# Optimization experiments

Measured on AMD Instinct MI355X. Metric: run time of the kernel, lower is better.

Reference implementation:

```python
import jax, jax.numpy as jnp
import numpy as np

N, F_IN, F_OUT = 8192, 256, 128
ALPHA = 0.2  # LeakyReLU negative slope
NEG_BIG = -9e15


def setup_inputs() -> dict:
    key = jax.random.key(0)
    k1, k2, k3, k4 = jax.random.split(key, 4)
    h = jax.random.normal(k1, (N, F_IN), dtype=jnp.float32)
    adj = jax.random.randint(k2, (N, N), 0, 2, dtype=jnp.int32)
    # Xavier-uniform-ish scaled params (gain 1.414)
    w_bound = 1.414 * np.sqrt(6.0 / (F_IN + F_OUT))
    a_bound = 1.414 * np.sqrt(6.0 / (2 * F_OUT + 1))
    W = jax.random.uniform(k3, (F_IN, F_OUT), jnp.float32, -w_bound, w_bound)
    a = jax.random.uniform(k4, (2 * F_OUT, 1), jnp.float32, -a_bound, a_bound)
    return {"h": h, "adj": adj, "W": W, "a": a}


def reference(h, adj, W, a):
    # Wh: [N, F_OUT]
    Wh = h @ W
    # a = [a1; a2]; e_ij = leakyrelu(a1.Wh_i + a2.Wh_j) == the torch concat+matmul,
    # computed via broadcast-add instead of materializing [N, N, 2F].
    a1 = a[:F_OUT, 0]   # [F_OUT]
    a2 = a[F_OUT:, 0]   # [F_OUT]
    si = Wh @ a1        # [N]
    sj = Wh @ a2        # [N]
    e = jax.nn.leaky_relu(si[:, None] + sj[None, :], negative_slope=ALPHA)  # [N, N]
    logits = jnp.where(adj > 0, e, NEG_BIG)
    attention = jax.nn.softmax(logits, axis=1)
    # dropout is identity in eval mode (training=False)
    h_prime = attention @ Wh  # [N, F_OUT]
    return jax.nn.elu(h_prime)  # concat=True path
```

## Files before the change

kernel.cpp:

```cpp
#include <hip/hip_runtime.h>

#define NN 8192
#define FIN 256
#define FOUT 128
#define BKJ 128
#define LALPHA 0.2f

typedef short bf16x8 __attribute__((ext_vector_type(8)));
typedef float f32x4 __attribute__((ext_vector_type(4)));

#define FOR8(X) X(0) X(1) X(2) X(3) X(4) X(5) X(6) X(7)

static __device__ __forceinline__ unsigned short f2bf(float f) {
    unsigned u = __float_as_uint(f);
    u += 0x7FFFu + ((u >> 16) & 1u);
    return (unsigned short)(u >> 16);
}
static __device__ __forceinline__ float bf2f(unsigned short b) {
    return __uint_as_float(((unsigned)b) << 16);
}

__global__ __launch_bounds__(256) void gat_k1(
    const float* __restrict__ h, const float* __restrict__ W,
    const float* __restrict__ a, unsigned short* __restrict__ WhT,
    float* __restrict__ si, float* __restrict__ sj)
{
    __shared__ float Wt[64 * 128];
    __shared__ float hT[64 * 36 + 4];
    const int t = threadIdx.x;
    const int r0 = blockIdx.x * 32;
    const int rg = t >> 5;
    const int cg = t & 31;
    float acc[4][4] = {{0.f,0.f,0.f,0.f},{0.f,0.f,0.f,0.f},{0.f,0.f,0.f,0.f},{0.f,0.f,0.f,0.f}};

    for (int kc = 0; kc < 4; ++kc) {
        __syncthreads();
        const float4* Ws = (const float4*)(W + kc * 64 * FOUT);
        float4* Wd = (float4*)Wt;
        #pragma unroll
        for (int v = 0; v < 8; ++v) Wd[v * 256 + t] = Ws[v * 256 + t];
        {
            const int hr = t >> 3, hk = (t & 7) * 8;
            const float* hs = h + (size_t)(r0 + hr) * FIN + kc * 64 + hk;
            float4 x0 = *(const float4*)hs;
            float4 x1 = *(const float4*)(hs + 4);
            hT[(hk + 0) * 36 + hr] = x0.x; hT[(hk + 1) * 36 + hr] = x0.y;
            hT[(hk + 2) * 36 + hr] = x0.z; hT[(hk + 3) * 36 + hr] = x0.w;
            hT[(hk + 4) * 36 + hr] = x1.x; hT[(hk + 5) * 36 + hr] = x1.y;
            hT[(hk + 6) * 36 + hr] = x1.z; hT[(hk + 7) * 36 + hr] = x1.w;
        }
        __syncthreads();
        #pragma unroll 8
        for (int kk = 0; kk < 64; ++kk) {
            float4 hv4 = *(const float4*)&hT[kk * 36 + rg * 4];
            float4 wv4 = *(const float4*)&Wt[kk * 128 + cg * 4];
            float hv[4] = {hv4.x, hv4.y, hv4.z, hv4.w};
            float wv[4] = {wv4.x, wv4.y, wv4.z, wv4.w};
            #pragma unroll
            for (int rr = 0; rr < 4; ++rr)
                #pragma unroll
                for (int cc = 0; cc < 4; ++cc)
                    acc[rr][cc] = fmaf(hv[rr], wv[cc], acc[rr][cc]);
        }
    }
    float4 a1v4 = *(const float4*)(a + cg * 4);
    float4 a2v4 = *(const float4*)(a + FOUT + cg * 4);
    float a1v[4] = {a1v4.x, a1v4.y, a1v4.z, a1v4.w};
    float a2v[4] = {a2v4.x, a2v4.y, a2v4.z, a2v4.w};
    float ps[4], qs[4];
    #pragma unroll
    for (int rr = 0; rr < 4; ++rr) {
        float p = 0.f, q = 0.f;
        #pragma unroll
        for (int cc = 0; cc < 4; ++cc) {
            p = fmaf(acc[rr][cc], a1v[cc], p);
            q = fmaf(acc[rr][cc], a2v[cc], q);
        }
        ps[rr] = p; qs[rr] = q;
    }
    #pragma unroll
    for (int off = 1; off <= 16; off <<= 1) {
        #pragma unroll
        for (int rr = 0; rr < 4; ++rr) {
            ps[rr] += __shfl_xor(ps[rr], off);
            qs[rr] += __shfl_xor(qs[rr], off);
        }
    }
    if (cg == 0) {
        #pragma unroll
        for (int rr = 0; rr < 4; ++rr) {
            si[r0 + rg * 4 + rr] = ps[rr];
            sj[r0 + rg * 4 + rr] = qs[rr];
        }
    }
    #pragma unroll
    for (int cc = 0; cc < 4; ++cc) {
        ushort4 v;
        v.x = f2bf(acc[0][cc]); v.y = f2bf(acc[1][cc]);
        v.z = f2bf(acc[2][cc]); v.w = f2bf(acc[3][cc]);
        *(ushort4*)(WhT + (size_t)(cg * 4 + cc) * NN + r0 + rg * 4) = v;
    }
}

__global__ __launch_bounds__(256) void gat_k1s(
    const float* __restrict__ sj, float* __restrict__ sjmax)
{
    __shared__ float red[256];
    float m = -1e30f;
    for (int i = threadIdx.x; i < NN; i += 256) m = fmaxf(m, sj[i]);
    red[threadIdx.x] = m;
    __syncthreads();
    for (int o = 128; o > 0; o >>= 1) {
        if (threadIdx.x < o) red[threadIdx.x] = fmaxf(red[threadIdx.x], red[threadIdx.x + o]);
        __syncthreads();
    }
    if (threadIdx.x == 0) sjmax[0] = red[0];
}

static __device__ __forceinline__ unsigned short pcalc(
    int a, float sjv, float si_l, float m_row, float& ls)
{
    float x = si_l + sjv;
    x = fmaxf(x, LALPHA * x);
    float p = (a > 0) ? __expf(x - m_row) : 0.f;
    unsigned short pb = f2bf(p);
    ls += bf2f(pb);
    return pb;
}

template<int JS, bool FINAL>
__global__ __launch_bounds__(256, 2) void gat_k2(
    const int* __restrict__ adj, const unsigned short* __restrict__ WhT,
    const float* __restrict__ si, const float* __restrict__ sj,
    const float* __restrict__ sjmaxp,
    float* __restrict__ lsum, float* __restrict__ Opart, float* __restrict__ out)
{
    const int JR_ = NN / JS;
    const int NST_ = JR_ / BKJ;
    __shared__ __align__(16) unsigned short tile[2][16384];
    const int t = threadIdx.x;
    const int w = t >> 6, l = t & 63;
    const int rb = (int)blockIdx.x / JS, js = (int)blockIdx.x % JS;
    const int iw = rb * 64 + w * 16;
    const int j0 = js * JR_;
    const int row = l & 15, kg = l >> 4;

    const float si_l = si[iw + row];
    const float sjmax = sjmaxp[0];
    const float xm = si_l + sjmax;
    const float m_row = fmaxf(xm, LALPHA * xm);
    const float* sjb = sj + j0 + kg * 8;
    const int c_row = t >> 4, ch = t & 15;
    const int* adjb = adj + (size_t)(iw + row) * NN + j0 + kg * 8;

#define GSRC_D(v) const unsigned short* gsrc##v = WhT + (size_t)(v * 16 + c_row) * NN + j0 + ch * 8; \
                  const int ldo##v = ((v * 256 + t) * 16) ^ ((c_row & 7) << 4);
    FOR8(GSRC_D)

#define REG_D(v) int4 stg##v, adr##v;
    FOR8(REG_D)

#define STG_L0(v) stg##v = *(const int4*)(gsrc##v);
    FOR8(STG_L0)
#define ADR_L0(q) adr##q = *(const int4*)(adjb + (q / 2) * 32 + (q % 2) * 4);
    FOR8(ADR_L0)

#define ACC_D(n) f32x4 acc##n = {0.f, 0.f, 0.f, 0.f};
    FOR8(ACC_D)
    float ls = 0.f;
    const int kg16 = kg * 16;

#define STG_WR(v) *(int4*)((char*)tb + ldo##v) = stg##v;
#define STG_LN(v) stg##v = *(const int4*)(gsrc##v + so);
#define ADR_LN(q) adr##q = *(const int4*)(adjb + so + (q / 2) * 32 + (q % 2) * 4);
#define P8(AF, A0, A1, sp) { \
    float4 s0_ = *(const float4*)(sp); float4 s1_ = *(const float4*)((sp) + 4); \
    AF[0] = (short)pcalc(A0.x, s0_.x, si_l, m_row, ls); \
    AF[1] = (short)pcalc(A0.y, s0_.y, si_l, m_row, ls); \
    AF[2] = (short)pcalc(A0.z, s0_.z, si_l, m_row, ls); \
    AF[3] = (short)pcalc(A0.w, s0_.w, si_l, m_row, ls); \
    AF[4] = (short)pcalc(A1.x, s1_.x, si_l, m_row, ls); \
    AF[5] = (short)pcalc(A1.y, s1_.y, si_l, m_row, ls); \
    AF[6] = (short)pcalc(A1.z, s1_.z, si_l, m_row, ls); \
    AF[7] = (short)pcalc(A1.w, s1_.w, si_l, m_row, ls); }
#define MFMA_ROW(n) { const int c_ = n * 16 + row; \
    const int off_ = c_ * 256 + (KB ^ ((c_ & 7) << 4)); \
    bf16x8 bv_ = *(const bf16x8*)((const char*)tb + off_); \
    acc##n = __builtin_amdgcn_mfma_f32_16x16x32_bf16(AFk, bv_, acc##n, 0, 0, 0); }
#define MFMA_KC(afv, kcl) { const bf16x8 AFk = afv; const int KB = kcl * 64 + kg16; FOR8(MFMA_ROW) }

    for (int s = 0; s < NST_; ++s) {
        unsigned short* tb = tile[s & 1];
        FOR8(STG_WR)
        if (s + 1 < NST_) {
            const size_t so = (size_t)(s + 1) * BKJ;
            FOR8(STG_LN)
        }
        bf16x8 af0, af1, af2, af3;
        {
            const float* spp = sjb + s * BKJ;
            P8(af0, adr0, adr1, spp)
            P8(af1, adr2, adr3, spp + 32)
            P8(af2, adr4, adr5, spp + 64)
            P8(af3, adr6, adr7, spp + 96)
        }
        if (s + 1 < NST_) {
            const size_t so = (size_t)(s + 1) * BKJ;
            FOR8(ADR_LN)
        }
        __syncthreads();
        MFMA_KC(af0, 0) MFMA_KC(af1, 1) MFMA_KC(af2, 2) MFMA_KC(af3, 3)
    }

    ls += __shfl_xor(ls, 16);
    ls += __shfl_xor(ls, 32);
    if (FINAL) {
        float lsr0 = __shfl(ls, kg * 4 + 0);
        float lsr1 = __shfl(ls, kg * 4 + 1);
        float lsr2 = __shfl(ls, kg * 4 + 2);
        float lsr3 = __shfl(ls, kg * 4 + 3);
#define FN_ROW(n) { size_t ob = (size_t)(iw + kg * 4) * FOUT + n * 16 + row; \
    float o0 = acc##n[0] / lsr0; out[ob]            = (o0 > 0.f) ? o0 : expm1f(o0); \
    float o1 = acc##n[1] / lsr1; out[ob + FOUT]     = (o1 > 0.f) ? o1 : expm1f(o1); \
    float o2 = acc##n[2] / lsr2; out[ob + 2 * FOUT] = (o2 > 0.f) ? o2 : expm1f(o2); \
    float o3 = acc##n[3] / lsr3; out[ob + 3 * FOUT] = (o3 > 0.f) ? o3 : expm1f(o3); }
        FOR8(FN_ROW)
    } else {
        if (l < 16) lsum[(size_t)js * NN + iw + l] = ls;
#define ST_ROW(n) { size_t ob = ((size_t)js * NN + iw + kg * 4) * FOUT + n * 16 + row; \
    Opart[ob] = acc##n[0]; Opart[ob + FOUT] = acc##n[1]; \
    Opart[ob + 2 * FOUT] = acc##n[2]; Opart[ob + 3 * FOUT] = acc##n[3]; }
        FOR8(ST_ROW)
    }
}

__global__ __launch_bounds__(256) void gat_k3(
    const float* __restrict__ lsum, const float* __restrict__ Opart,
    float* __restrict__ out)
{
    const int t = threadIdx.x;
    const int i = (int)blockIdx.x * 2 + (t >> 7);
    const int f = t & 127;
    float den = lsum[i] + lsum[NN + i] + lsum[2 * NN + i] + lsum[3 * NN + i];
    size_t base = (size_t)i * FOUT + f;
    const size_t SP = (size_t)NN * FOUT;
    float num = Opart[base] + Opart[SP + base]
              + Opart[2 * SP + base] + Opart[3 * SP + base];
    float o = num / den;
    out[base] = (o > 0.f) ? o : expm1f(o);
}

extern "C" void kernel_launch(void* const* d_in, const int* in_sizes, int n_in,
                              void* d_out, int out_size, void* d_ws, size_t ws_size,
                              hipStream_t stream) {
    const float* h  = (const float*)d_in[0];
    const int*  adj = (const int*)d_in[1];
    const float* W  = (const float*)d_in[2];
    const float* a  = (const float*)d_in[3];
    float* out = (float*)d_out;
    char* ws = (char*)d_ws;
    unsigned short* WhT = (unsigned short*)ws;
    float* si     = (float*)(ws + 2097152);
    float* sj     = (float*)(ws + 2129920);
    float* sjmax  = (float*)(ws + 2162688);
    float* lsum   = (float*)(ws + 2162944);
    float* Opart  = (float*)(ws + 2294016);
    const size_t need4 = 2294016 + (size_t)4 * NN * FOUT * 4;

    gat_k1<<<256, 256, 0, stream>>>(h, W, a, WhT, si, sj);
    gat_k1s<<<1, 256, 0, stream>>>(sj, sjmax);
    if (ws_size >= need4) {
        gat_k2<4, false><<<512, 256, 0, stream>>>(adj, WhT, si, sj, sjmax, lsum, Opart, out);
        gat_k3<<<4096, 256, 0, stream>>>(lsum, Opart, out);
    } else {
        gat_k2<1, true><<<128, 256, 0, stream>>>(adj, WhT, si, sj, sjmax, lsum, Opart, out);
    }
}
```

Before: 98.58 us.

## Load WhT MFMA operands directly from global memory, removing LDS tile staging

Drops the double-buffered shared-memory tile and __syncthreads. Each lane now loads its B-fragments of WhT straight from global memory into registers, split into two batches around the softmax-probability computation. The row-sum accumulator is split into four independent partial sums to shorten the dependency chain. This removes LDS traffic and block-wide barriers but makes each wave fetch WhT separately (4 waves per block now load the same data), uses more VGPRs, and relies on L2/L1 hits.

```diff
diff --git a/kernel.cpp b/kernel.cpp
--- a/kernel.cpp
+++ b/kernel.cpp
@@ -137,7 +137,6 @@
 {
     const int JR_ = NN / JS;
     const int NST_ = JR_ / BKJ;
-    __shared__ __align__(16) unsigned short tile[2][16384];
     const int t = threadIdx.x;
     const int w = t >> 6, l = t & 63;
     const int rb = (int)blockIdx.x / JS, js = (int)blockIdx.x % JS;
@@ -150,68 +149,66 @@
     const float xm = si_l + sjmax;
     const float m_row = fmaxf(xm, LALPHA * xm);
     const float* sjb = sj + j0 + kg * 8;
-    const int c_row = t >> 4, ch = t & 15;
     const int* adjb = adj + (size_t)(iw + row) * NN + j0 + kg * 8;
 
-#define GSRC_D(v) const unsigned short* gsrc##v = WhT + (size_t)(v * 16 + c_row) * NN + j0 + ch * 8; \
-                  const int ldo##v = ((v * 256 + t) * 16) ^ ((c_row & 7) << 4);
-    FOR8(GSRC_D)
-
-#define REG_D(v) int4 stg##v, adr##v;
-    FOR8(REG_D)
-
-#define STG_L0(v) stg##v = *(const int4*)(gsrc##v);
-    FOR8(STG_L0)
+#define WB_D(n) const unsigned short* wb##n = WhT + (size_t)(n * 16 + row) * NN + j0 + kg * 8;
+    FOR8(WB_D)
+
+#define ADR_D(q) int4 adr##q;
+    FOR8(ADR_D)
 #define ADR_L0(q) adr##q = *(const int4*)(adjb + (q / 2) * 32 + (q % 2) * 4);
     FOR8(ADR_L0)
 
 #define ACC_D(n) f32x4 acc##n = {0.f, 0.f, 0.f, 0.f};
     FOR8(ACC_D)
-    float ls = 0.f;
-    const int kg16 = kg * 16;
-
-#define STG_WR(v) *(int4*)((char*)tb + ldo##v) = stg##v;
-#define STG_LN(v) stg##v = *(const int4*)(gsrc##v + so);
+    float ls0 = 0.f, ls1 = 0.f, ls2 = 0.f, ls3 = 0.f;
+
 #define ADR_LN(q) adr##q = *(const int4*)(adjb + so + (q / 2) * 32 + (q % 2) * 4);
-#define P8(AF, A0, A1, sp) { \
+#define P8(AF, A0, A1, sp, LSV) { \
     float4 s0_ = *(const float4*)(sp); float4 s1_ = *(const float4*)((sp) + 4); \
-    AF[0] = (short)pcalc(A0.x, s0_.x, si_l, m_row, ls); \
-    AF[1] = (short)pcalc(A0.y, s0_.y, si_l, m_row, ls); \
-    AF[2] = (short)pcalc(A0.z, s0_.z, si_l, m_row, ls); \
-    AF[3] = (short)pcalc(A0.w, s0_.w, si_l, m_row, ls); \
-    AF[4] = (short)pcalc(A1.x, s1_.x, si_l, m_row, ls); \
-    AF[5] = (short)pcalc(A1.y, s1_.y, si_l, m_row, ls); \
-    AF[6] = (short)pcalc(A1.z, s1_.z, si_l, m_row, ls); \
-    AF[7] = (short)pcalc(A1.w, s1_.w, si_l, m_row, ls); }
-#define MFMA_ROW(n) { const int c_ = n * 16 + row; \
-    const int off_ = c_ * 256 + (KB ^ ((c_ & 7) << 4)); \
-    bf16x8 bv_ = *(const bf16x8*)((const char*)tb + off_); \
-    acc##n = __builtin_amdgcn_mfma_f32_16x16x32_bf16(AFk, bv_, acc##n, 0, 0, 0); }
-#define MFMA_KC(afv, kcl) { const bf16x8 AFk = afv; const int KB = kcl * 64 + kg16; FOR8(MFMA_ROW) }
-
+    AF[0] = (short)pcalc(A0.x, s0_.x, si_l, m_row, LSV); \
+    AF[1] = (short)pcalc(A0.y, s0_.y, si_l, m_row, LSV); \
+    AF[2] = (short)pcalc(A0.z, s0_.z, si_l, m_row, LSV); \
+    AF[3] = (short)pcalc(A0.w, s0_.w, si_l, m_row, LSV); \
+    AF[4] = (short)pcalc(A1.x, s1_.x, si_l, m_row, LSV); \
+    AF[5] = (short)pcalc(A1.y, s1_.y, si_l, m_row, LSV); \
+    AF[6] = (short)pcalc(A1.z, s1_.z, si_l, m_row, LSV); \
+    AF[7] = (short)pcalc(A1.w, s1_.w, si_l, m_row, LSV); }
+#define FG_L0(n) int4 fg0##n = *(const int4*)(wb##n + sofs);
+#define FG_L1(n) int4 fg1##n = *(const int4*)(wb##n + sofs + 32);
+#define FG_L2(n) int4 fg2##n = *(const int4*)(wb##n + sofs + 64);
+#define FG_L3(n) int4 fg3##n = *(const int4*)(wb##n + sofs + 96);
+#define MM0(n) acc##n = __builtin_amdgcn_mfma_f32_16x16x32_bf16(af0, *(const bf16x8*)&fg0##n, acc##n, 0, 0, 0);
+#define MM1(n) acc##n = __builtin_amdgcn_mfma_f32_16x16x32_bf16(af1, *(const bf16x8*)&fg1##n, acc##n, 0, 0, 0);
+#define MM2(n) acc##n = __builtin_amdgcn_mfma_f32_16x16x32_bf16(af2, *(const bf16x8*)&fg2##n, acc##n, 0, 0, 0);
+#define MM3(n) acc##n = __builtin_amdgcn_mfma_f32_16x16x32_bf16(af3, *(const bf16x8*)&fg3##n, acc##n, 0, 0, 0);
+
+    #pragma unroll 1
     for (int s = 0; s < NST_; ++s) {
-        unsigned short* tb = tile[s & 1];
-        FOR8(STG_WR)
-        if (s + 1 < NST_) {
-            const size_t so = (size_t)(s + 1) * BKJ;
-            FOR8(STG_LN)
-        }
+        const size_t sofs = (size_t)s * BKJ;
+        FOR8(FG_L0)
+        FOR8(FG_L1)
         bf16x8 af0, af1, af2, af3;
         {
             const float* spp = sjb + s * BKJ;
-            P8(af0, adr0, adr1, spp)
-            P8(af1, adr2, adr3, spp + 32)
-            P8(af2, adr4, adr5, spp + 64)
-            P8(af3, adr6, adr7, spp + 96)
+            P8(af0, adr0, adr1, spp,      ls0)
+            P8(af1, adr2, adr3, spp + 32, ls1)
+            P8(af2, adr4, adr5, spp + 64, ls2)
+            P8(af3, adr6, adr7, spp + 96, ls3)
         }
         if (s + 1 < NST_) {
             const size_t so = (size_t)(s + 1) * BKJ;
             FOR8(ADR_LN)
         }
-        __syncthreads();
-        MFMA_KC(af0, 0) MFMA_KC(af1, 1) MFMA_KC(af2, 2) MFMA_KC(af3, 3)
-    }
-
+        FOR8(FG_L2)
+        FOR8(FG_L3)
+        FOR8(MM0)
+        FOR8(MM1)
+        FOR8(MM2)
+        FOR8(MM3)
+    }
+
+    float ls = (ls0 + ls1) + (ls2 + ls3);
     ls += __shfl_xor(ls, 16);
     ls += __shfl_xor(ls, 32);
     if (FINAL) {
```

Result: slower. 184.3 us (+86.9%).

## Halve j-tile, double split-K to 8, compute row sums via MFMA with ones

Applied to the files above, without the earlier changes.

Shrinks the per-stage j tile from 128 to 64 to halve LDS and register staging, which allows four blocks per CU, and doubles the j-split to eight so 1024 blocks cover the GPU. The softmax denominator is no longer accumulated with scalar adds and shuffles. It comes from an extra MFMA against a vector of bf16 ones, taking VALU work off the exp path. The trade-off is twice as much partial-output traffic written and then reduced in gat_k3, plus a larger workspace.

```diff
diff --git a/kernel.cpp b/kernel.cpp
--- a/kernel.cpp
+++ b/kernel.cpp
@@ -3,21 +3,20 @@
 #define NN 8192
 #define FIN 256
 #define FOUT 128
-#define BKJ 128
+#define BKJ 64
+#define JSPLIT 8
 #define LALPHA 0.2f
 
 typedef short bf16x8 __attribute__((ext_vector_type(8)));
 typedef float f32x4 __attribute__((ext_vector_type(4)));
 
 #define FOR8(X) X(0) X(1) X(2) X(3) X(4) X(5) X(6) X(7)
+#define FOR4(X) X(0) X(1) X(2) X(3)
 
 static __device__ __forceinline__ unsigned short f2bf(float f) {
     unsigned u = __float_as_uint(f);
     u += 0x7FFFu + ((u >> 16) & 1u);
     return (unsigned short)(u >> 16);
-}
-static __device__ __forceinline__ float bf2f(unsigned short b) {
-    return __uint_as_float(((unsigned)b) << 16);
 }
 
 __global__ __launch_bounds__(256) void gat_k1(
@@ -118,18 +117,16 @@
 }
 
 static __device__ __forceinline__ unsigned short pcalc(
-    int a, float sjv, float si_l, float m_row, float& ls)
+    int a, float sjv, float si_l, float m_row)
 {
     float x = si_l + sjv;
     x = fmaxf(x, LALPHA * x);
     float p = (a > 0) ? __expf(x - m_row) : 0.f;
-    unsigned short pb = f2bf(p);
-    ls += bf2f(pb);
-    return pb;
+    return f2bf(p);
 }
 
 template<int JS, bool FINAL>
-__global__ __launch_bounds__(256, 2) void gat_k2(
+__global__ __launch_bounds__(256, 4) void gat_k2(
     const int* __restrict__ adj, const unsigned short* __restrict__ WhT,
     const float* __restrict__ si, const float* __restrict__ sj,
     const float* __restrict__ sjmaxp,
@@ -137,7 +134,7 @@
 {
     const int JR_ = NN / JS;
     const int NST_ = JR_ / BKJ;
-    __shared__ __align__(16) unsigned short tile[2][16384];
+    __shared__ __align__(16) unsigned short tile[2][8192];
     const int t = threadIdx.x;
     const int w = t >> 6, l = t & 63;
     const int rb = (int)blockIdx.x / JS, js = (int)blockIdx.x % JS;
@@ -150,24 +147,25 @@
     const float xm = si_l + sjmax;
     const float m_row = fmaxf(xm, LALPHA * xm);
     const float* sjb = sj + j0 + kg * 8;
-    const int c_row = t >> 4, ch = t & 15;
     const int* adjb = adj + (size_t)(iw + row) * NN + j0 + kg * 8;
 
-#define GSRC_D(v) const unsigned short* gsrc##v = WhT + (size_t)(v * 16 + c_row) * NN + j0 + ch * 8; \
-                  const int ldo##v = ((v * 256 + t) * 16) ^ ((c_row & 7) << 4);
-    FOR8(GSRC_D)
+#define GSRC_D(v) const unsigned short* gsrc##v = WhT + (size_t)(v * 32 + (t >> 3)) * NN + j0 + (t & 7) * 8; \
+                  const int ldo##v = ((v * 256 + t) * 16) ^ (((t >> 3) & 7) << 4);
+    FOR4(GSRC_D)
 
 #define REG_D(v) int4 stg##v, adr##v;
-    FOR8(REG_D)
-
+    FOR4(REG_D)
 #define STG_L0(v) stg##v = *(const int4*)(gsrc##v);
-    FOR8(STG_L0)
+    FOR4(STG_L0)
 #define ADR_L0(q) adr##q = *(const int4*)(adjb + (q / 2) * 32 + (q % 2) * 4);
-    FOR8(ADR_L0)
+    FOR4(ADR_L0)
 
 #define ACC_D(n) f32x4 acc##n = {0.f, 0.f, 0.f, 0.f};
     FOR8(ACC_D)
-    float ls = 0.f;
+    f32x4 acc8 = {0.f, 0.f, 0.f, 0.f};
+    bf16x8 ones;
+    #pragma unroll
+    for (int z = 0; z < 8; ++z) ones[z] = (short)0x3F80;
     const int kg16 = kg * 16;
 
 #define STG_WR(v) *(int4*)((char*)tb + ldo##v) = stg##v;
@@ -175,58 +173,55 @@
 #define ADR_LN(q) adr##q = *(const int4*)(adjb + so + (q / 2) * 32 + (q % 2) * 4);
 #define P8(AF, A0, A1, sp) { \
     float4 s0_ = *(const float4*)(sp); float4 s1_ = *(const float4*)((sp) + 4); \
-    AF[0] = (short)pcalc(A0.x, s0_.x, si_l, m_row, ls); \
-    AF[1] = (short)pcalc(A0.y, s0_.y, si_l, m_row, ls); \
-    AF[2] = (short)pcalc(A0.z, s0_.z, si_l, m_row, ls); \
-    AF[3] = (short)pcalc(A0.w, s0_.w, si_l, m_row, ls); \
-    AF[4] = (short)pcalc(A1.x, s1_.x, si_l, m_row, ls); \
-    AF[5] = (short)pcalc(A1.y, s1_.y, si_l, m_row, ls); \
-    AF[6] = (short)pcalc(A1.z, s1_.z, si_l, m_row, ls); \
-    AF[7] = (short)pcalc(A1.w, s1_.w, si_l, m_row, ls); }
+    AF[0] = (short)pcalc(A0.x, s0_.x, si_l, m_row); \
+    AF[1] = (short)pcalc(A0.y, s0_.y, si_l, m_row); \
+    AF[2] = (short)pcalc(A0.z, s0_.z, si_l, m_row); \
+    AF[3] = (short)pcalc(A0.w, s0_.w, si_l, m_row); \
+    AF[4] = (short)pcalc(A1.x, s1_.x, si_l, m_row); \
+    AF[5] = (short)pcalc(A1.y, s1_.y, si_l, m_row); \
+    AF[6] = (short)pcalc(A1.z, s1_.z, si_l, m_row); \
+    AF[7] = (short)pcalc(A1.w, s1_.w, si_l, m_row); }
 #define MFMA_ROW(n) { const int c_ = n * 16 + row; \
-    const int off_ = c_ * 256 + (KB ^ ((c_ & 7) << 4)); \
+    const int off_ = c_ * 128 + ((KB ^ ((c_ & 7) << 4))); \
     bf16x8 bv_ = *(const bf16x8*)((const char*)tb + off_); \
     acc##n = __builtin_amdgcn_mfma_f32_16x16x32_bf16(AFk, bv_, acc##n, 0, 0, 0); }
-#define MFMA_KC(afv, kcl) { const bf16x8 AFk = afv; const int KB = kcl * 64 + kg16; FOR8(MFMA_ROW) }
+#define MFMA_KC(afv, kcl) { const bf16x8 AFk = afv; const int KB = kcl * 64 + kg16; FOR8(MFMA_ROW) \
+    acc8 = __builtin_amdgcn_mfma_f32_16x16x32_bf16(AFk, ones, acc8, 0, 0, 0); }
 
     for (int s = 0; s < NST_; ++s) {
         unsigned short* tb = tile[s & 1];
-        FOR8(STG_WR)
+        FOR4(STG_WR)
         if (s + 1 < NST_) {
             const size_t so = (size_t)(s + 1) * BKJ;
-            FOR8(STG_LN)
-        }
-        bf16x8 af0, af1, af2, af3;
+            FOR4(STG_LN)
+        }
+        bf16x8 af0, af1;
         {
             const float* spp = sjb + s * BKJ;
             P8(af0, adr0, adr1, spp)
             P8(af1, adr2, adr3, spp + 32)
-            P8(af2, adr4, adr5, spp + 64)
-            P8(af3, adr6, adr7, spp + 96)
         }
         if (s + 1 < NST_) {
             const size_t so = (size_t)(s + 1) * BKJ;
-            FOR8(ADR_LN)
-        }
-        __syncthreads();
-        MFMA_KC(af0, 0) MFMA_KC(af1, 1) MFMA_KC(af2, 2) MFMA_KC(af3, 3)
-    }
-
-    ls += __shfl_xor(ls, 16);
-    ls += __shfl_xor(ls, 32);
+            FOR4(ADR_LN)
+        }
+        __syncthreads();
+        MFMA_KC(af0, 0) MFMA_KC(af1, 1)
+    }
+
     if (FINAL) {
-        float lsr0 = __shfl(ls, kg * 4 + 0);
-        float lsr1 = __shfl(ls, kg * 4 + 1);
-        float lsr2 = __shfl(ls, kg * 4 + 2);
-        float lsr3 = __shfl(ls, kg * 4 + 3);
 #define FN_ROW(n) { size_t ob = (size_t)(iw + kg * 4) * FOUT + n * 16 + row; \
-    float o0 = acc##n[0] / lsr0; out[ob]            = (o0 > 0.f) ? o0 : expm1f(o0); \
-    float o1 = acc##n[1] / lsr1; out[ob + FOUT]     = (o1 > 0.f) ? o1 : expm1f(o1); \
-    float o2 = acc##n[2] / lsr2; out[ob + 2 * FOUT] = (o2 > 0.f) ? o2 : expm1f(o2); \
-    float o3 = acc##n[3] / lsr3; out[ob + 3 * FOUT] = (o3 > 0.f) ? o3 : expm1f(o3); }
+    float o0 = acc##n[0] / acc8[0]; out[ob]            = (o0 > 0.f) ? o0 : expm1f(o0); \
+    float o1 = acc##n[1] / acc8[1]; out[ob + FOUT]     = (o1 > 0.f) ? o1 : expm1f(o1); \
+    float o2 = acc##n[2] / acc8[2]; out[ob + 2 * FOUT] = (o2 > 0.f) ? o2 : expm1f(o2); \
+    float o3 = acc##n[3] / acc8[3]; out[ob + 3 * FOUT] = (o3 > 0.f) ? o3 : expm1f(o3); }
         FOR8(FN_ROW)
     } else {
-        if (l < 16) lsum[(size_t)js * NN + iw + l] = ls;
+        if (row == 0) {
+            #pragma unroll
+            for (int q = 0; q < 4; ++q)
+                lsum[(size_t)js * NN + iw + kg * 4 + q] = acc8[q];
+        }
 #define ST_ROW(n) { size_t ob = ((size_t)js * NN + iw + kg * 4) * FOUT + n * 16 + row; \
     Opart[ob] = acc##n[0]; Opart[ob + FOUT] = acc##n[1]; \
     Opart[ob + 2 * FOUT] = acc##n[2]; Opart[ob + 3 * FOUT] = acc##n[3]; }
@@ -241,11 +236,14 @@
     const int t = threadIdx.x;
     const int i = (int)blockIdx.x * 2 + (t >> 7);
     const int f = t & 127;
-    float den = lsum[i] + lsum[NN + i] + lsum[2 * NN + i] + lsum[3 * NN + i];
+    float den = 0.f, num = 0.f;
+    const size_t SP = (size_t)NN * FOUT;
     size_t base = (size_t)i * FOUT + f;
-    const size_t SP = (size_t)NN * FOUT;
-    float num = Opart[base] + Opart[SP + base]
-              + Opart[2 * SP + base] + Opart[3 * SP + base];
+    #pragma unroll
+    for (int k = 0; k < JSPLIT; ++k) {
+        den += lsum[(size_t)k * NN + i];
+        num += Opart[(size_t)k * SP + base];
+    }
     float o = num / den;
     out[base] = (o > 0.f) ? o : expm1f(o);
 }
@@ -264,13 +262,13 @@
     float* sj     = (float*)(ws + 2129920);
     float* sjmax  = (float*)(ws + 2162688);
     float* lsum   = (float*)(ws + 2162944);
-    float* Opart  = (float*)(ws + 2294016);
-    const size_t need4 = 2294016 + (size_t)4 * NN * FOUT * 4;
+    float* Opart  = (float*)(ws + 2425088);
+    const size_t need = 2425088 + (size_t)JSPLIT * NN * FOUT * 4;
 
     gat_k1<<<256, 256, 0, stream>>>(h, W, a, WhT, si, sj);
     gat_k1s<<<1, 256, 0, stream>>>(sj, sjmax);
-    if (ws_size >= need4) {
-        gat_k2<4, false><<<512, 256, 0, stream>>>(adj, WhT, si, sj, sjmax, lsum, Opart, out);
+    if (ws_size >= need) {
+        gat_k2<JSPLIT, false><<<128 * JSPLIT, 256, 0, stream>>>(adj, WhT, si, sj, sjmax, lsum, Opart, out);
         gat_k3<<<4096, 256, 0, stream>>>(lsum, Opart, out);
     } else {
         gat_k2<1, true><<<128, 256, 0, stream>>>(adj, WhT, si, sj, sjmax, lsum, Opart, out);
```

New measurement: 111.1 us. 1.13x slower.
